# Optimization experiments

Measured on AMD Instinct MI355X. Metric: run time of the kernel, lower is better.

The kernel has to match this reference:

```python
import jax, jax.numpy as jnp
import numpy as np

NF = 64
DG = 8
NB = 5
K = 3
K2 = K * K


def conv2d(x, w, b):
    # x: [B,C,H,W], w: [O,I,3,3] -> SAME padding, stride 1
    y = jax.lax.conv_general_dilated(x, w, (1, 1), 'SAME',
                                     dimension_numbers=('NCHW', 'OIHW', 'NCHW'))
    return y + b[None, :, None, None]


def dcn(x, off_feat, cw, cb, w, b):
    """Modulated deformable conv (DCNv2, extra_offset_mask=True).
    x: [B,C,H,W] sampled input; off_feat: [B,C,H,W] feeds conv_offset_mask.
    cw/cb: offset-mask conv params [3*DG*K2, C, 3, 3]; w/b: main conv [O, C, 3, 3].
    """
    B, C, H, W = x.shape
    Cg = C // DG
    om = conv2d(off_feat, cw, cb)                      # [B, 3*DG*K2, H, W]
    o1, o2, m = jnp.split(om, 3, axis=1)
    dy = o1.reshape(B, DG, K2, H, W)
    dx = o2.reshape(B, DG, K2, H, W)
    mask = jax.nn.sigmoid(m).reshape(B, DG, K2, H, W)
    # kernel tap offsets for 3x3, pad=1, dilation=1
    kyy, kxx = np.meshgrid(np.arange(K) - 1, np.arange(K) - 1, indexing='ij')
    ky = jnp.asarray(kyy.reshape(K2), x.dtype)
    kx = jnp.asarray(kxx.reshape(K2), x.dtype)
    gy = jnp.arange(H, dtype=x.dtype)
    gx = jnp.arange(W, dtype=x.dtype)
    py = gy[None, None, None, :, None] + ky[None, None, :, None, None] + dy  # [B,DG,K2,H,W]
    px = gx[None, None, None, None, :] + kx[None, None, :, None, None] + dx
    y0 = jnp.floor(py)
    x0 = jnp.floor(px)
    wy = py - y0
    wx = px - x0
    y0i = y0.astype(jnp.int32)
    x0i = x0.astype(jnp.int32)
    xg = x.reshape(B, DG, Cg, H * W)

    def gather(iy, ix):
        valid = ((iy >= 0) & (iy < H) & (ix >= 0) & (ix < W)).astype(x.dtype)
        lin = (jnp.clip(iy, 0, H - 1) * W + jnp.clip(ix, 0, W - 1)).reshape(B, DG, 1, K2 * H * W)
        v = jnp.take_along_axis(xg, jnp.broadcast_to(lin, (B, DG, Cg, K2 * H * W)), axis=3)
        return v.reshape(B, DG, Cg, K2, H, W) * valid[:, :, None]

    v00 = gather(y0i, x0i)
    v01 = gather(y0i, x0i + 1)
    v10 = gather(y0i + 1, x0i)
    v11 = gather(y0i + 1, x0i + 1)
    wy_ = wy[:, :, None]
    wx_ = wx[:, :, None]
    val = (v00 * (1 - wy_) * (1 - wx_) + v01 * (1 - wy_) * wx_
           + v10 * wy_ * (1 - wx_) + v11 * wy_ * wx_) * mask[:, :, None]  # [B,DG,Cg,K2,H,W]
    wr = w.reshape(w.shape[0], DG, Cg, K2)
    out = jnp.einsum('bgckhw,ogck->bohw', val, wr) + b[None, :, None, None]
    return out


def setup_inputs() -> dict:
    key = jax.random.key(0)
    ks = jax.random.split(key, 16)

    def w_(k, shape, s=0.05):
        return jax.random.normal(k, shape, jnp.float32) * s

    B, N, C, H, W = 4, 5, 1, 128, 128
    inp = {}
    inp['x'] = jax.random.normal(ks[0], (B, N, C, H, W), jnp.float32)
    inp['w_init'] = w_(ks[1], (NF, C, 3, 3))
    inp['b_init'] = jnp.zeros((NF,), jnp.float32)
    inp['res_w1'] = w_(ks[2], (NB, NF, NF, 3, 3))
    inp['res_b1'] = jnp.zeros((NB, NF), jnp.float32)
    inp['res_w2'] = w_(ks[3], (NB, NF, NF, 3, 3))
    inp['res_b2'] = jnp.zeros((NB, NF), jnp.float32)
    inp['w_bn'] = w_(ks[4], (NF, 2 * NF, 3, 3))
    inp['b_bn'] = jnp.zeros((NF,), jnp.float32)
    inp['off_w'] = w_(ks[5], (4, NF, NF, 3, 3))
    inp['off_b'] = jnp.zeros((4, NF), jnp.float32)
    inp['com_w'] = w_(ks[6], (4, 3 * DG * K2, NF, 3, 3), 0.01)
    inp['com_b'] = jnp.zeros((4, 3 * DG * K2), jnp.float32)
    inp['dcn_w'] = w_(ks[7], (4, NF, NF, 3, 3))
    inp['dcn_b'] = jnp.zeros((4, NF), jnp.float32)
    inp['w_rec'] = w_(ks[8], (C, NF, 3, 3))
    inp['b_rec'] = jnp.zeros((C,), jnp.float32)
    return inp


def reference(x, w_init, b_init, res_w1, res_b1, res_w2, res_b2, w_bn, b_bn,
              off_w, off_b, com_w, com_b, dcn_w, dcn_b, w_rec, b_rec):
    B, N, C, H, W = x.shape
    y = x.reshape(B * N, C, H, W)
    out = jax.nn.relu(conv2d(y, w_init, b_init))
    for i in range(NB):  # ResidualBlock_noBN x nb
        h = jax.nn.relu(conv2d(out, res_w1[i], res_b1[i]))
        out = out + conv2d(h, res_w2[i], res_b2[i])
    out = out.reshape(B, N, NF, H, W)
    ref = out[:, N // 2]
    ys = []
    for i in range(N):
        nei = out[:, i]
        fea = conv2d(jnp.concatenate([ref, nei], axis=1), w_bn, b_bn)
        o = conv2d(fea, off_w[0], off_b[0])
        fea = dcn(fea, o, com_w[0], com_b[0], dcn_w[0], dcn_b[0])
        o = conv2d(fea, off_w[1], off_b[1])
        fea = dcn(fea, o, com_w[1], com_b[1], dcn_w[1], dcn_b[1])
        o = conv2d(fea, off_w[2], off_b[2])
        fea = dcn(nei, o, com_w[2], com_b[2], dcn_w[2], dcn_b[2])
        o = conv2d(fea, off_w[3], off_b[3])
        aligned = dcn(fea, o, com_w[3], com_b[3], dcn_w[3], dcn_b[3])
        ys.append(conv2d(aligned, w_rec, b_rec))
    return jnp.concatenate(ys, axis=1)  # [B, N*C, H, W]
```

## Files before the change

### kernel.cpp

```cpp
#include <hip/hip_runtime.h>
#include <hip/hip_bf16.h>

typedef __hip_bfloat16 bf16;
typedef __attribute__((ext_vector_type(8))) short short8;
typedef __attribute__((ext_vector_type(4))) float floatx4;
typedef unsigned short ush;

#define HH 128
#define WW 128
#define HW 16384

__device__ __forceinline__ float b2f(bf16 v){ return __bfloat162float(v); }
__device__ __forceinline__ float bfu2f(ush u){
  union{unsigned int i; float f;} c; c.i = ((unsigned int)u)<<16; return c.f;
}
__device__ __forceinline__ ush f2bfu(float f){
  bf16 h = __float2bfloat16(f);
  return *(ush*)&h;
}

__global__ void detect_dtype(const ush* __restrict__ x, float* __restrict__ flag){
  __shared__ int bad;
  if (threadIdx.x==0) bad = 0;
  __syncthreads();
  for (int j=threadIdx.x; j<4096; j+=256){
    float f = bfu2f(x[j]);
    if (!(fabsf(f) < 1e4f)) atomicOr(&bad, 1);
  }
  __syncthreads();
  if (threadIdx.x==0) flag[0] = bad ? 0.f : 1.f;
}

__global__ void convert_in(const void* __restrict__ src, float* __restrict__ dst, int n,
                           const float* __restrict__ flag){
  int i = blockIdx.x*256 + threadIdx.x;
  if (i >= n) return;
  float v = (flag[0] > 0.5f) ? b2f(((const bf16*)src)[i]) : ((const float*)src)[i];
  dst[i] = v;
}

__global__ void transpose_w(const float* __restrict__ src, float* __restrict__ dst, int Co, int CiK){
  int tid = blockIdx.x*256 + threadIdx.x;
  if (tid >= Co*CiK) return;
  int co = tid / CiK, r = tid - co*CiK;
  dst[(long)r*Co + co] = src[tid];
}

__global__ void pack_w2(const float* __restrict__ src, ush* __restrict__ dst,
                        int Cout, int Cin, int kh, int nOcB){
  int idx = blockIdx.x*256 + threadIdx.x;
  int total = nOcB*36864;
  if (idx >= total) return;
  int ocb = idx / 36864; int r = idx - ocb*36864;
  int c  = r & 7;
  int lx = (r>>3) & 15;
  int n  = (r>>7) & 3;
  int lk = (r>>9) & 3;
  int j  = r>>11;
  int t = j>>1, ch = j&1;
  int oc = n*16+lx;
  int k = ch*32 + lk*8 + c;
  int ocg = ocb*64 + oc, icg = kh*64 + k;
  float v = (ocg < Cout && icg < Cin) ? src[((long)ocg*Cin + icg)*9 + t] : 0.f;
  dst[idx] = f2bfu(v);
}

__global__ void pack_dcn_w(const float* __restrict__ src, ush* __restrict__ dst){
  int idx = blockIdx.x*256 + threadIdx.x;
  if (idx >= 49152) return;
  int g = idx / 6144; int r = idx - g*6144;
  int oc = r / 96; int k = r - oc*96;
  float v = 0.f;
  if (k < 72){
    int tap = k >> 3, c = k & 7;
    v = src[((long)oc*64 + g*8 + c)*9 + tap];
  }
  dst[idx] = f2bfu(v);
}

__global__ __launch_bounds__(256) void conv_init_kernel(const float* __restrict__ x,
    const float* __restrict__ wT, const float* __restrict__ bias,
    ush* __restrict__ fh, ush* __restrict__ fl){
  __shared__ ush L[256*66];
  int tid = threadIdx.x;
  int tx = tid & 15, ty = tid >> 4;
  int gx = blockIdx.x*16+tx, gy = blockIdx.y*16+ty;
  int n = blockIdx.z;
  const float* xp = x + (long)n*HW;
  float v[9];
  #pragma unroll
  for (int dy=0;dy<3;dy++)
    #pragma unroll
    for (int dx=0;dx<3;dx++){
      int yy = gy+dy-1, xx = gx+dx-1;
      bool ok = (yy>=0)&&(yy<HH)&&(xx>=0)&&(xx<WW);
      v[dy*3+dx] = ok ? xp[yy*WW+xx] : 0.f;
    }
  float acc[64];
  #pragma unroll 1
  for (int oc=0; oc<64; oc++){
    float a = bias[oc];
    #pragma unroll
    for (int k=0;k<9;k++) a = fmaf(v[k], wT[k*64+oc], a);
    acc[oc] = fmaxf(a, 0.f);
  }
  #pragma unroll 1
  for (int pass=0; pass<2; pass++){
    #pragma unroll 1
    for (int oc=0; oc<64; oc++){
      float a = acc[oc];
      ush h = f2bfu(a);
      L[tid*66+oc] = pass ? f2bfu(a - bfu2f(h)) : h;
    }
    __syncthreads();
    ush* dst = pass ? fl : fh;
    for (int j=tid; j<2048; j+=256){
      int c8 = j&7, pidx = j>>3;
      int row = pidx>>4, col = pidx&15;
      long addr = ((long)n*HW + (blockIdx.y*16+row)*WW + blockIdx.x*16+col)*64 + c8*8;
      *(short8*)(dst+addr) = *(const short8*)(L + pidx*66 + c8*8);
    }
    __syncthreads();
  }
}

template<int NPL, int MINW, int MT>
__global__ __launch_bounds__(256, MINW) void conv_mfma(
    const ush* __restrict__ in_hi, const ush* __restrict__ in_lo, long in_ps,
    const ush* __restrict__ in2_hi, const ush* __restrict__ in2_lo, long in2_ps,
    const ush* __restrict__ wpack, const ush* __restrict__ wpack2,
    const float* __restrict__ bias, int has_bias,
    const ush* __restrict__ add_hi, const ush* __restrict__ add_lo,
    long add_ps, int add_cs,
    ush* __restrict__ out_hi, ush* __restrict__ out_lo,
    long out_ps, int out_cs,
    ush* __restrict__ out_pb, int pf_C,
    int Cout, int nOcB, int relu)
{
  constexpr int ROWS = 4*MT + 2;
  constexpr int APX  = ROWS*18;
  constexpr int NPX  = 4*MT*16;
  constexpr int LDSN = (NPL*APX*64 > 2*NPX*66) ? NPL*APX*64 : 2*NPX*66;
  __shared__ ush A[LDSN];
  int tid = threadIdx.x;
  int z = blockIdx.z; int img = z / nOcB; int ocb = z - img*nOcB;
  int x0 = blockIdx.x*16 - 1, y0 = blockIdx.y*(4*MT) - 1;
  int w = tid>>6, l = tid&63, lx = l&15, lk = l>>4;
  floatx4 acc[MT][4];
  #pragma unroll
  for (int mt=0;mt<MT;mt++)
    #pragma unroll
    for (int n=0;n<4;n++) acc[mt][n] = (floatx4){0.f,0.f,0.f,0.f};

  auto phase = [&](const ush* ihb, const ush* ilb, const ush* wfb){
    __syncthreads();
    #pragma unroll
    for (int p=0;p<NPL;p++){
      const ush* src = p ? ilb : ihb;
      ush* dstp = A + p*APX*64;
      for (int j=tid; j<APX*8; j+=256){
        int pidx = j>>3, c8 = j&7;
        int row = pidx/18, col = pidx - row*18;
        int yy = y0+row, xx = x0+col;
        uint4 v = make_uint4(0u,0u,0u,0u);
        if ((unsigned)yy < 128u && (unsigned)xx < 128u)
          v = *(const uint4*)(src + ((long)(yy*WW+xx))*64 + c8*8);
        *(uint4*)(dstp + pidx*64 + ((c8 ^ (pidx&7))<<3)) = v;
      }
    }
    const ush* wfrag = wfb + lk*4*128 + lx*8;
    short8 bf[4][4];
    #pragma unroll
    for (int s=0;s<3;s++)
      #pragma unroll
      for (int n=0;n<4;n++)
        bf[s][n] = *(const short8*)(wfrag + (s*16 + n)*128);
    __syncthreads();
    #pragma unroll
    for (int j=0;j<18;j++){
      int t = j>>1, ch = j&1;
      if (j<15){
        #pragma unroll
        for (int n=0;n<4;n++)
          bf[(j+3)&3][n] = *(const short8*)(wfrag + ((j+3)*16 + n)*128);
      }
      int ky = t/3, kx = t - ky*3;
      int jc = ch*4 + lk;
      #pragma unroll
      for (int mt=0; mt<MT; mt++){
        int pidx = (w*MT+mt+ky)*18 + lx + kx;
        #pragma unroll
        for (int p=0;p<NPL;p++){
          short8 af = *(const short8*)(A + p*APX*64 + pidx*64 + ((jc ^ (pidx&7))<<3));
          #pragma unroll
          for (int n=0;n<4;n++)
            acc[mt][n] = __builtin_amdgcn_mfma_f32_16x16x32_bf16(af, bf[j&3][n], acc[mt][n], 0,0,0);
        }
      }
    }
  };
  phase(in_hi + (long)img*in_ps*64, in_lo + (long)img*in_ps*64,
        wpack + (long)ocb*36864);
  if (wpack2)
    phase(in2_hi + (long)img*in2_ps*64, in2_lo + (long)img*in2_ps*64,
          wpack2 + (long)ocb*36864);

  int ybase = blockIdx.y*(4*MT) + w*MT;
  int xbase = blockIdx.x*16 + lk*4;
  if (out_pb){
    #pragma unroll
    for (int mt=0;mt<MT;mt++){
      int y = ybase + mt;
      #pragma unroll
      for (int n=0;n<4;n++){
        int ocg = ocb*64 + n*16 + lx;
        if (ocg < Cout){
          float bv = has_bias ? bias[ocg] : 0.f;
          #pragma unroll
          for (int r=0;r<4;r++){
            int xg = xbase + r;
            out_pb[((long)img*pf_C + ocg)*HW + y*WW + xg] = f2bfu(acc[mt][n][r] + bv);
          }
        }
      }
    }
  } else {
    __syncthreads();
    ush* L0 = A;
    ush* L1 = A + NPX*66;
    #pragma unroll
    for (int mt=0;mt<MT;mt++){
      int y = ybase + mt;
      int rowl = w*MT + mt;
      #pragma unroll
      for (int n=0;n<4;n++){
        int ocg = n*16 + lx;
        float bv = has_bias ? bias[ocg] : 0.f;
        #pragma unroll
        for (int r=0;r<4;r++){
          int coll = lk*4 + r;
          float v = acc[mt][n][r] + bv;
          if (add_hi){
            long ap = ((long)img*add_ps + y*WW + blockIdx.x*16 + coll)*add_cs + ocg;
            v += bfu2f(add_hi[ap]) + bfu2f(add_lo[ap]);
          }
          if (relu) v = fmaxf(v, 0.f);
          ush h = f2bfu(v);
          L0[(rowl*16+coll)*66 + ocg] = h;
          if (out_lo) L1[(rowl*16+coll)*66 + ocg] = f2bfu(v - bfu2f(h));
        }
      }
    }
    __syncthreads();
    for (int j=tid; j<NPX*8; j+=256){
      int pidx = j>>3, c8 = j&7;
      int row = pidx>>4, col = pidx&15;
      long pp = (long)img*out_ps + (blockIdx.y*(4*MT)+row)*WW + blockIdx.x*16+col;
      *(short8*)(out_hi + pp*64 + c8*8) = *(const short8*)(L0 + pidx*66 + c8*8);
      if (out_lo)
        *(short8*)(out_lo + pp*64 + c8*8) = *(const short8*)(L1 + pidx*66 + c8*8);
    }
  }
}

__global__ __launch_bounds__(256,4) void res_fused(
    const ush* __restrict__ src_h, const ush* __restrict__ src_l,
    const ush* __restrict__ w1, const float* __restrict__ b1,
    const ush* __restrict__ w2, const float* __restrict__ b2,
    ush* __restrict__ dst_h, ush* __restrict__ dst_l)
{
  __shared__ ush F[180*64];
  __shared__ ush Hs[112*64];
  int tid = threadIdx.x;
  int bx = blockIdx.x, by = blockIdx.y, img = blockIdx.z;
  int fy0 = by*4 - 2, fx0 = bx*16 - 2;
  int w = tid>>6, l = tid&63, lx = l&15, lk = l>>4;
  const ush* sh = src_h + (long)img*HW*64;
  for (int j=tid; j<1440; j+=256){
    int pidx = j>>3, c8 = j&7;
    int row = pidx/20, col = pidx - row*20;
    int yy = fy0+row, xx = fx0+col;
    uint4 v = make_uint4(0u,0u,0u,0u);
    if ((unsigned)yy<128u && (unsigned)xx<128u)
      v = *(const uint4*)(sh + ((long)(yy*WW+xx))*64 + c8*8);
    *(uint4*)(F + pidx*64 + ((c8 ^ (pidx&7))<<3)) = v;
  }
  const ush* wf1 = w1 + lk*4*128 + lx*8;
  int hrow[2], hcol[2], hvalid[2];
  #pragma unroll
  for (int mm=0;mm<2;mm++){
    int m = w + mm*4;
    hvalid[mm] = (m < 7);
    int hp = m*16 + lx;
    hrow[mm] = hp/18; hcol[mm] = hp - hrow[mm]*18;
  }
  floatx4 acc1[2][4];
  #pragma unroll
  for (int mm=0;mm<2;mm++)
    #pragma unroll
    for (int n=0;n<4;n++) acc1[mm][n] = (floatx4){0.f,0.f,0.f,0.f};
  short8 bf[4][4];
  #pragma unroll
  for (int s=0;s<3;s++)
    #pragma unroll
    for (int n=0;n<4;n++)
      bf[s][n] = *(const short8*)(wf1 + (s*16 + n)*128);
  __syncthreads();
  #pragma unroll
  for (int j=0;j<18;j++){
    int t = j>>1, ch = j&1;
    if (j<15){
      #pragma unroll
      for (int n=0;n<4;n++)
        bf[(j+3)&3][n] = *(const short8*)(wf1 + ((j+3)*16 + n)*128);
    }
    int ky = t/3, kx = t - ky*3;
    int jc = ch*4 + lk;
    #pragma unroll
    for (int mm=0;mm<2;mm++){
      if (!hvalid[mm]) continue;
      int pidx = (hrow[mm]+ky)*20 + hcol[mm] + kx;
      short8 af = *(const short8*)(F + pidx*64 + ((jc ^ (pidx&7))<<3));
      #pragma unroll
      for (int n=0;n<4;n++)
        acc1[mm][n] = __builtin_amdgcn_mfma_f32_16x16x32_bf16(af, bf[j&3][n], acc1[mm][n], 0,0,0);
    }
  }
  #pragma unroll
  for (int mm=0;mm<2;mm++){
    if (!hvalid[mm]) continue;
    int m = w + mm*4;
    #pragma unroll
    for (int n=0;n<4;n++){
      int oc = n*16+lx;
      float bv = b1[oc];
      #pragma unroll
      for (int r=0;r<4;r++){
        int hp = m*16 + lk*4 + r;
        int hr = hp/18, hc = hp - hr*18;
        int fy = fy0 + 1 + hr, fx = fx0 + 1 + hc;
        bool inimg = ((unsigned)fy < 128u) && ((unsigned)fx < 128u);
        float v = inimg ? fmaxf(acc1[mm][n][r] + bv, 0.f) : 0.f;
        Hs[hp*64 + (((oc>>3) ^ (hp&7))<<3) + (oc&7)] = f2bfu(v);
      }
    }
  }
  __syncthreads();
  const ush* wf2 = w2 + lk*4*128 + lx*8;
  floatx4 acc2[4];
  #pragma unroll
  for (int n=0;n<4;n++) acc2[n] = (floatx4){0.f,0.f,0.f,0.f};
  #pragma unroll
  for (int s=0;s<3;s++)
    #pragma unroll
    for (int n=0;n<4;n++)
      bf[s][n] = *(const short8*)(wf2 + (s*16 + n)*128);
  #pragma unroll
  for (int j=0;j<18;j++){
    int t = j>>1, ch = j&1;
    if (j<15){
      #pragma unroll
      for (int n=0;n<4;n++)
        bf[(j+3)&3][n] = *(const short8*)(wf2 + ((j+3)*16 + n)*128);
    }
    int ky = t/3, kx = t - ky*3;
    int jc = ch*4 + lk;
    int pidx = (w+ky)*18 + lx + kx;
    short8 af = *(const short8*)(Hs + pidx*64 + ((jc ^ (pidx&7))<<3));
    #pragma unroll
    for (int n=0;n<4;n++)
      acc2[n] = __builtin_amdgcn_mfma_f32_16x16x32_bf16(af, bf[j&3][n], acc2[n], 0,0,0);
  }
  const ush* sl = src_l + (long)img*HW*64;
  int gy = by*4 + w;
  float vout[4][4];
  #pragma unroll
  for (int n=0;n<4;n++){
    int oc = n*16+lx;
    float bv = b2[oc];
    #pragma unroll
    for (int r=0;r<4;r++){
      int colp = lk*4 + r;
      int gx = bx*16 + colp;
      int pt = (w+2)*20 + colp + 2;
      float fh = bfu2f(F[pt*64 + (((oc>>3) ^ (pt&7))<<3) + (oc&7)]);
      float fl = bfu2f(sl[((long)(gy*WW+gx))*64 + oc]);
      vout[n][r] = acc2[n][r] + bv + fh + fl;
    }
  }
  __syncthreads();
  ush* L0 = F;
  ush* L1 = F + 64*66;
  #pragma unroll
  for (int n=0;n<4;n++){
    int oc = n*16+lx;
    #pragma unroll
    for (int r=0;r<4;r++){
      int px = w*16 + lk*4 + r;
      float v = vout[n][r];
      ush h = f2bfu(v);
      L0[px*66 + oc] = h;
      L1[px*66 + oc] = f2bfu(v - bfu2f(h));
    }
  }
  __syncthreads();
  for (int j=tid; j<512; j+=256){
    int pidx = j>>3, c8 = j&7;
    int row = pidx>>4, col = pidx&15;
    long pp = ((long)img*HW + (by*4+row)*WW + bx*16+col)*64 + c8*8;
    *(short8*)(dst_h + pp) = *(const short8*)(L0 + pidx*66 + c8*8);
    *(short8*)(dst_l + pp) = *(const short8*)(L1 + pidx*66 + c8*8);
  }
}

__global__ __launch_bounds__(256) void repack_gp(const ush* __restrict__ in_h,
    const ush* __restrict__ in_l, long in_ps, ush* __restrict__ gp){
  long idx = (long)blockIdx.x*256 + threadIdx.x;
  int img = (int)(idx >> 17);
  int rem = (int)(idx & 131071);
  int pix = rem >> 3, c8 = rem & 7;
  long src = ((long)img*in_ps + pix)*64 + c8*8;
  short8 h = *(const short8*)(in_h+src);
  short8 lo = *(const short8*)(in_l+src);
  short8 o;
  #pragma unroll
  for (int c=0;c<8;c++) o[c] = (short)f2bfu(bfu2f((ush)h[c]) + bfu2f((ush)lo[c]));
  *(short8*)(gp + (((long)(img*8+c8))*HW + pix)*8) = o;
}

__global__ __launch_bounds__(256) void dcn_mfma(
    const ush* __restrict__ gp,
    const ush* __restrict__ om,
    const ush* __restrict__ wpk,
    const float* __restrict__ bias,
    ush* __restrict__ out_hi, ush* __restrict__ out_lo)
{
  __shared__ ush S[13312];
  ush* Ah = S;
  ush* Bt = S + 6656;
  int tid = threadIdx.x;
  int half = blockIdx.x, gy = blockIdx.y, img = blockIdx.z;
  int xoff = half*64;
  {
    short8 z = {0,0,0,0,0,0,0,0};
    for (int j=tid; j<192; j+=256){
      int px = j/3, c = j - px*3;
      *(short8*)(Ah + px*104 + 72 + c*8) = z;
    }
  }
  int w = tid>>6, l = tid&63, lx = l&15, lk = l>>4;
  int px_s = tid & 63, q = tid >> 6;
  int t0 = (q==0)?0:(q*2+1), t1 = t0 + ((q==0)?3:2);
  const ush* omb = om + (long)img*216*HW + gy*WW + xoff + px_s;
  floatx4 acc[4];
  #pragma unroll
  for (int n=0;n<4;n++) acc[n] = (floatx4){0.f,0.f,0.f,0.f};

  #pragma unroll 1
  for (int g=0; g<8; g++){
    __syncthreads();
    const ush* wsrc = wpk + g*6144;
    for (int j=tid; j<768; j+=256){
      int oc = j/12, kc = j - oc*12;
      *(short8*)(Bt + oc*104 + kc*8) = *(const short8*)(wsrc + oc*96 + kc*8);
    }
    const ush* gpb = gp + ((long)(img*8+g))*HW*8;
    #pragma unroll 1
    for (int t=t0; t<t1; t++){
      int ch = g*9+t;
      float dy = bfu2f(omb[(long)ch*HW]);
      float dx = bfu2f(omb[(long)(72+ch)*HW]);
      float mv = bfu2f(omb[(long)(144+ch)*HW]);
      float m = 1.f/(1.f+__expf(-mv));
      float py = (float)gy + (float)(t/3 - 1) + dy;
      float pxf = (float)(xoff + px_s) + (float)(t%3 - 1) + dx;
      float fy = floorf(py), fx = floorf(pxf);
      int y0 = (int)fy, x0 = (int)fx;
      float wy = py - fy, wx = pxf - fx;
      bool y0v = (y0>=0 && y0<HH), y1v = (y0+1>=0 && y0+1<HH);
      bool x0v = (x0>=0 && x0<WW), x1v = (x0+1>=0 && x0+1<WW);
      float w00 = (1.f-wy)*(1.f-wx)*m * ((y0v&&x0v)?1.f:0.f);
      float w01 = (1.f-wy)*wx*m      * ((y0v&&x1v)?1.f:0.f);
      float w10 = wy*(1.f-wx)*m      * ((y1v&&x0v)?1.f:0.f);
      float w11 = wy*wx*m            * ((y1v&&x1v)?1.f:0.f);
      int y0c = min(max(y0,0),HH-1), y1c = min(max(y0+1,0),HH-1);
      int x0c = min(max(x0,0),WW-1), x1c = min(max(x0+1,0),WW-1);
      short8 s00 = *(const short8*)(gpb + (((long)(y0c*WW+x0c))<<3));
      short8 s01 = *(const short8*)(gpb + (((long)(y0c*WW+x1c))<<3));
      short8 s10 = *(const short8*)(gpb + (((long)(y1c*WW+x0c))<<3));
      short8 s11 = *(const short8*)(gpb + (((long)(y1c*WW+x1c))<<3));
      short8 vh;
      #pragma unroll
      for (int c=0;c<8;c++){
        float val = w00*bfu2f((ush)s00[c]) + w01*bfu2f((ush)s01[c])
                  + w10*bfu2f((ush)s10[c]) + w11*bfu2f((ush)s11[c]);
        vh[c] = (short)f2bfu(val);
      }
      *(short8*)(Ah + px_s*104 + t*8) = vh;
    }
    __syncthreads();
    #pragma unroll
    for (int ks=0; ks<3; ks++){
      short8 bfg[4];
      #pragma unroll
      for (int n=0;n<4;n++)
        bfg[n] = *(const short8*)(Bt + (n*16+lx)*104 + ks*32 + lk*8);
      int px = w*16 + lx;
      short8 ah = *(const short8*)(Ah + px*104 + ks*32 + lk*8);
      #pragma unroll
      for (int n=0;n<4;n++)
        acc[n] = __builtin_amdgcn_mfma_f32_16x16x32_bf16(ah, bfg[n], acc[n], 0,0,0);
    }
  }
  __syncthreads();
  ush* L0 = S;
  ush* L1 = S + 64*66;
  #pragma unroll
  for (int n=0;n<4;n++){
    int oc = n*16 + lx;
    float bv = bias[oc];
    #pragma unroll
    for (int r=0;r<4;r++){
      int pxl = w*16 + lk*4 + r;
      float v = acc[n][r] + bv;
      ush h = f2bfu(v);
      L0[pxl*66 + oc] = h;
      L1[pxl*66 + oc] = f2bfu(v - bfu2f(h));
    }
  }
  __syncthreads();
  long base = ((long)img*HW + gy*WW + xoff)*64;
  for (int j=tid; j<512; j+=256){
    int pidx = j>>3, c8 = j&7;
    *(short8*)(out_hi + base + pidx*64 + c8*8) = *(const short8*)(L0 + pidx*66 + c8*8);
    *(short8*)(out_lo + base + pidx*64 + c8*8) = *(const short8*)(L1 + pidx*66 + c8*8);
  }
}

__global__ __launch_bounds__(256) void rec_kernel(
    const ush* __restrict__ fh, const ush* __restrict__ fl,
    const float* __restrict__ wT, const float* __restrict__ bias,
    void* __restrict__ out, int ni, const float* __restrict__ flag){
  __shared__ float red[256];
  int tid = threadIdx.x;
  int p = tid & 31, q = tid >> 5;
  int gx = blockIdx.x*32 + p;
  int gy = blockIdx.y;
  int b = blockIdx.z;
  float acc = 0.f;
  #pragma unroll
  for (int t=0;t<9;t++){
    int yy = gy + t/3 - 1, xx = gx + t%3 - 1;
    if (yy<0||yy>=HH||xx<0||xx>=WW) continue;
    long base = ((long)b*HW + yy*WW + xx)*64 + q*8;
    short8 h = *(const short8*)(fh + base);
    short8 lo = *(const short8*)(fl + base);
    #pragma unroll
    for (int cc=0;cc<8;cc++){
      float v = bfu2f((ush)h[cc]) + bfu2f((ush)lo[cc]);
      acc = fmaf(v, wT[(q*8+cc)*9 + t], acc);
    }
  }
  red[q*32+p] = acc;
  __syncthreads();
  if (tid < 32){
    float s = bias[0];
    #pragma unroll
    for (int k=0;k<8;k++) s += red[k*32+tid];
    long idx = ((long)b*5+ni)*HW + gy*WW + blockIdx.x*32 + tid;
    if (flag[0] > 0.5f) ((bf16*)out)[idx] = __float2bfloat16(s);
    else                ((float*)out)[idx] = s;
  }
}

extern "C" void kernel_launch(void* const* d_in, const int* in_sizes, int n_in,
                              void* d_out, int out_size, void* d_ws, size_t ws_size,
                              hipStream_t stream) {
  float* ws = (float*)d_ws;

  size_t off = 16;
  auto alloc = [&](size_t nel){ size_t o = off; off += (nel + 7) & ~(size_t)7; return o; };

  static const int IN_N[17] = {327680, 576, 64, 184320, 320, 184320, 320,
                               73728, 64, 147456, 256, 497664, 864, 147456,
                               256, 576, 1};
  size_t cin[17];
  for (int i=0;i<17;i++) cin[i] = alloc(IN_N[i]);

  size_t wt_init = alloc(640);
  size_t wdcn_pk[4]; for (int s=0;s<4;s++) wdcn_pk[s] = alloc(24576);
  size_t wt_rec = alloc(640);
  size_t pk_res1[5], pk_res2[5];
  for (int i=0;i<5;i++) pk_res1[i] = alloc(18432);
  for (int i=0;i<5;i++) pk_res2[i] = alloc(18432);
  size_t pk_bn[2]; for (int h=0;h<2;h++) pk_bn[h] = alloc(18432);
  size_t pk_off[4]; for (int s=0;s<4;s++) pk_off[s] = alloc(18432);
  size_t pk_com[4]; for (int s=0;s<4;s++) pk_com[s] = alloc(73728);

  size_t feat_h_o = alloc(10485760);
  size_t feat_l_o = alloc(10485760);
  size_t U = alloc(26738688);

  ush* feat_h = (ush*)(ws + feat_h_o);
  ush* feat_l = (ush*)(ws + feat_l_o);
  ush* alt_h  = (ush*)(ws + U);
  ush* alt_l  = (ush*)(ws + U + 10485760);
  ush* hbuf_h = (ush*)(ws + U + 10485760);
  ush* feaA_h = (ush*)(ws + U);
  ush* feaA_l = (ush*)(ws + U + 2097152);
  ush* feaB_h = (ush*)(ws + U + 4194304);
  ush* feaB_l = (ush*)(ws + U + 6291456);
  ush* obuf_h = (ush*)(ws + U + 8388608);
  ush* gpbuf  = (ush*)(ws + U + 10485760);
  ush* ombuf  = (ush*)(ws + U + 12582912);

  float* flag = ws;

  detect_dtype<<<dim3(1), dim3(256), 0, stream>>>((const ush*)d_in[0], flag);
  for (int i=0;i<17;i++){
    int n = IN_N[i];
    convert_in<<<dim3((n+255)/256), dim3(256), 0, stream>>>(d_in[i], ws+cin[i], n, flag);
  }
  const float* b_init = ws+cin[2];
  const float* res_b1 = ws+cin[4];
  const float* res_b2 = ws+cin[6];
  const float* b_bn   = ws+cin[8];
  const float* off_b  = ws+cin[10];
  const float* com_b  = ws+cin[12];
  const float* dcn_b  = ws+cin[14];
  const float* b_rec  = ws+cin[16];

  auto tr = [&](size_t src_o, size_t dst_o, int Co, int CiK){
    int total = Co*CiK;
    transpose_w<<<dim3((total+255)/256), dim3(256), 0, stream>>>(ws+src_o, ws+dst_o, Co, CiK);
  };
  tr(cin[1], wt_init, 64, 9);
  tr(cin[15], wt_rec, 1, 576);
  for (int s=0;s<4;s++)
    pack_dcn_w<<<dim3(192), dim3(256), 0, stream>>>(ws+cin[13]+(size_t)s*36864,
                                                    (ush*)(ws+wdcn_pk[s]));

  auto pack = [&](size_t src_o, size_t dst_o, int Cout, int Cin, int kh, int nOcB){
    int total = nOcB*36864;
    pack_w2<<<dim3((total+255)/256), dim3(256), 0, stream>>>(
        ws+src_o, (ush*)(ws+dst_o), Cout, Cin, kh, nOcB);
  };
  for (int i=0;i<5;i++) pack(cin[3]+(size_t)i*36864, pk_res1[i], 64, 64, 0, 1);
  for (int i=0;i<5;i++) pack(cin[5]+(size_t)i*36864, pk_res2[i], 64, 64, 0, 1);
  for (int h=0;h<2;h++) pack(cin[7], pk_bn[h], 64, 128, h, 1);
  for (int s=0;s<4;s++) pack(cin[9]+(size_t)s*36864,  pk_off[s], 64, 64, 0, 1);
  for (int s=0;s<4;s++) pack(cin[11]+(size_t)s*124416, pk_com[s], 216, 64, 0, 4);

  dim3 cblk(256);
  auto conv = [&](const ush* in_h, const ush* in_l, long in_ps,
                  const ush* in2_h, const ush* in2_l, long in2_ps,
                  size_t pk, const ush* pk2p,
                  const float* bias, int has_bias,
                  const ush* add_h, const ush* add_l, long add_ps, int add_cs,
                  ush* o_h, ush* o_l, long out_ps, int out_cs,
                  ush* o_pb, int pf_C,
                  int Cout, int nOcB, int relu, int N, int nPl, int mtMode){
    if (nPl == 2 && mtMode == 2)
      conv_mfma<2,2,2><<<dim3(8,16,N*nOcB), cblk, 0, stream>>>(
          in_h, in_l, in_ps, in2_h, in2_l, in2_ps,
          (const ush*)(ws+pk), pk2p, bias, has_bias,
          add_h, add_l, add_ps, add_cs, o_h, o_l, out_ps, out_cs,
          o_pb, pf_C, Cout, nOcB, relu);
    else if (nPl == 2 && mtMode == 1)
      conv_mfma<2,2,1><<<dim3(8,32,N*nOcB), cblk, 0, stream>>>(
          in_h, in_l, in_ps, in2_h, in2_l, in2_ps,
          (const ush*)(ws+pk), pk2p, bias, has_bias,
          add_h, add_l, add_ps, add_cs, o_h, o_l, out_ps, out_cs,
          o_pb, pf_C, Cout, nOcB, relu);
    else if (nPl == 1 && mtMode == 1)
      conv_mfma<1,3,1><<<dim3(8,32,N*nOcB), cblk, 0, stream>>>(
          in_h, in_l, in_ps, in2_h, in2_l, in2_ps,
          (const ush*)(ws+pk), pk2p, bias, has_bias,
          add_h, add_l, add_ps, add_cs, o_h, o_l, out_ps, out_cs,
          o_pb, pf_C, Cout, nOcB, relu);
    else
      conv_mfma<1,3,2><<<dim3(8,16,N*nOcB), cblk, 0, stream>>>(
          in_h, in_l, in_ps, in2_h, in2_l, in2_ps,
          (const ush*)(ws+pk), pk2p, bias, has_bias,
          add_h, add_l, add_ps, add_cs, o_h, o_l, out_ps, out_cs,
          o_pb, pf_C, Cout, nOcB, relu);
  };

  conv_init_kernel<<<dim3(8,8,20), cblk, 0, stream>>>(ws+cin[0], ws+wt_init, b_init,
                                                      feat_h, feat_l);
  conv(feat_h, feat_l, HW, nullptr, nullptr, 0, pk_res1[0], nullptr,
       res_b1, 1,
       nullptr, nullptr, 0, 0, hbuf_h, nullptr, HW, 64, nullptr, 0, 64, 1, 1, 20, 2, 1);
  conv(hbuf_h, hbuf_h, HW, nullptr, nullptr, 0, pk_res2[0], nullptr,
       res_b2, 1,
       feat_h, feat_l, HW, 64, feat_h, feat_l, HW, 64, nullptr, 0, 64, 1, 0, 20, 1, 1);
  {
    ush *sh = feat_h, *sl = feat_l, *dh = alt_h, *dl = alt_l;
    for (int i=1;i<5;i++){
      res_fused<<<dim3(8,32,20), cblk, 0, stream>>>(
          sh, sl, (const ush*)(ws+pk_res1[i]), res_b1+(size_t)i*64,
          (const ush*)(ws+pk_res2[i]), res_b2+(size_t)i*64, dh, dl);
      ush* t;
      t = sh; sh = dh; dh = t;
      t = sl; sl = dl; dl = t;
    }
  }
  for (int i=0;i<5;i++){
    conv(feat_h + (size_t)2*HW*64, feat_l + (size_t)2*HW*64, 5L*HW,
         feat_h + (size_t)i*HW*64, feat_l + (size_t)i*HW*64, 5L*HW,
         pk_bn[0], (const ush*)(ws+pk_bn[1]), b_bn, 1,
         nullptr, nullptr, 0, 0, feaA_h, feaA_l, HW, 64, nullptr, 0, 64, 1, 0, 4, 2, 1);
    ush *fa_h = feaA_h, *fa_l = feaA_l, *fb_h = feaB_h, *fb_l = feaB_l;
    for (int s=0;s<4;s++){
      conv(fa_h, fa_h, HW, nullptr, nullptr, 0, pk_off[s], nullptr,
           off_b+(size_t)s*64, 1,
           nullptr, nullptr, 0, 0, obuf_h, nullptr, HW, 64, nullptr, 0, 64, 1, 0, 4, 1, 1);
      conv(obuf_h, obuf_h, HW, nullptr, nullptr, 0, pk_com[s], nullptr,
           com_b+(size_t)s*216, 1,
           nullptr, nullptr, 0, 0, nullptr, nullptr, 0, 0, ombuf, 216, 216, 4, 0, 4, 1, 2);
      const ush *xs_h, *xs_l; long xps;
      if (s == 2){ xs_h = feat_h + (size_t)i*HW*64; xs_l = feat_l + (size_t)i*HW*64; xps = 5L*HW; }
      else       { xs_h = fa_h;                     xs_l = fa_l;                     xps = HW; }
      repack_gp<<<dim3(2048), cblk, 0, stream>>>(xs_h, xs_l, xps, gpbuf);
      dcn_mfma<<<dim3(2,128,4), cblk, 0, stream>>>(gpbuf, ombuf,
          (const ush*)(ws+wdcn_pk[s]), dcn_b+(size_t)s*64, fb_h, fb_l);
      ush* t;
      t = fa_h; fa_h = fb_h; fb_h = t;
      t = fa_l; fa_l = fb_l; fb_l = t;
    }
    rec_kernel<<<dim3(4,128,4), cblk, 0, stream>>>(fa_h, fa_l, ws+wt_rec, b_rec, d_out, i, flag);
  }
}
```

Before: 3.002 ms.

## Fuse gather-layout repack into producer epilogues and batch weight-prep launches

```diff
diff --git a/kernel.cpp b/kernel.cpp
--- a/kernel.cpp
+++ b/kernel.cpp
@@ -31,12 +31,17 @@
   if (threadIdx.x==0) flag[0] = bad ? 0.f : 1.f;
 }
 
-__global__ void convert_in(const void* __restrict__ src, float* __restrict__ dst, int n,
-                           const float* __restrict__ flag){
-  int i = blockIdx.x*256 + threadIdx.x;
-  if (i >= n) return;
-  float v = (flag[0] > 0.5f) ? b2f(((const bf16*)src)[i]) : ((const float*)src)[i];
-  dst[i] = v;
+struct CvtArgs { const void* src[17]; int dst[17]; };
+__global__ void convert_all(CvtArgs a, float* __restrict__ ws, const float* __restrict__ flag){
+  static const int N[17] = {327680, 576, 64, 184320, 320, 184320, 320,
+                            73728, 64, 147456, 256, 497664, 864, 147456,
+                            256, 576, 1};
+  int i = blockIdx.y;
+  int idx = blockIdx.x*256 + threadIdx.x;
+  if (idx >= N[i]) return;
+  float v = (flag[0] > 0.5f) ? b2f(((const bf16*)a.src[i])[idx])
+                             : ((const float*)a.src[i])[idx];
+  ws[a.dst[i] + idx] = v;
 }
 
 __global__ void transpose_w(const float* __restrict__ src, float* __restrict__ dst, int Co, int CiK){
@@ -46,11 +51,17 @@
   dst[(long)r*Co + co] = src[tid];
 }
 
-__global__ void pack_w2(const float* __restrict__ src, ush* __restrict__ dst,
-                        int Cout, int Cin, int kh, int nOcB){
+struct PackArgs { int src[20]; int dst[20]; short Cout[20]; short Cin[20];
+                  short kh[20]; short nOcB[20]; };
+__global__ void pack_all(PackArgs a, const float* __restrict__ ws, ush* __restrict__ wsu){
+  int jb = blockIdx.y;
   int idx = blockIdx.x*256 + threadIdx.x;
+  int nOcB = a.nOcB[jb];
   int total = nOcB*36864;
   if (idx >= total) return;
+  const float* src = ws + a.src[jb];
+  ush* dst = wsu + 2*(size_t)a.dst[jb];
+  int Cout = a.Cout[jb], Cin = a.Cin[jb], kh = a.kh[jb];
   int ocb = idx / 36864; int r = idx - ocb*36864;
   int c  = r & 7;
   int lx = (r>>3) & 15;
@@ -65,7 +76,10 @@
   dst[idx] = f2bfu(v);
 }
 
-__global__ void pack_dcn_w(const float* __restrict__ src, ush* __restrict__ dst){
+__global__ void pack_dcn_w(const float* __restrict__ src0, ush* __restrict__ dst0){
+  int s = blockIdx.y;
+  const float* src = src0 + (long)s*36864;
+  ush* dst = dst0 + (long)s*49152;
   int idx = blockIdx.x*256 + threadIdx.x;
   if (idx >= 49152) return;
   int g = idx / 6144; int r = idx - g*6144;
@@ -135,6 +149,7 @@
     ush* __restrict__ out_hi, ush* __restrict__ out_lo,
     long out_ps, int out_cs,
     ush* __restrict__ out_pb, int pf_C,
+    ush* __restrict__ gp_out,
     int Cout, int nOcB, int relu)
 {
   constexpr int ROWS = 4*MT + 2;
@@ -255,10 +270,21 @@
     for (int j=tid; j<NPX*8; j+=256){
       int pidx = j>>3, c8 = j&7;
       int row = pidx>>4, col = pidx&15;
-      long pp = (long)img*out_ps + (blockIdx.y*(4*MT)+row)*WW + blockIdx.x*16+col;
-      *(short8*)(out_hi + pp*64 + c8*8) = *(const short8*)(L0 + pidx*66 + c8*8);
-      if (out_lo)
-        *(short8*)(out_lo + pp*64 + c8*8) = *(const short8*)(L1 + pidx*66 + c8*8);
+      long pix = (blockIdx.y*(4*MT)+row)*WW + blockIdx.x*16+col;
+      long pp = (long)img*out_ps + pix;
+      short8 h8 = *(const short8*)(L0 + pidx*66 + c8*8);
+      *(short8*)(out_hi + pp*64 + c8*8) = h8;
+      if (out_lo){
+        short8 l8 = *(const short8*)(L1 + pidx*66 + c8*8);
+        *(short8*)(out_lo + pp*64 + c8*8) = l8;
+        if (gp_out){
+          short8 g;
+          #pragma unroll
+          for (int c=0;c<8;c++)
+            g[c] = (short)f2bfu(bfu2f((ush)h8[c]) + bfu2f((ush)l8[c]));
+          *(short8*)(gp_out + (((long)(img*8+c8))*HW + pix)*8) = g;
+        }
+      }
     }
   }
 }
@@ -433,7 +459,8 @@
     const ush* __restrict__ om,
     const ush* __restrict__ wpk,
     const float* __restrict__ bias,
-    ush* __restrict__ out_hi, ush* __restrict__ out_lo)
+    ush* __restrict__ out_hi, ush* __restrict__ out_lo,
+    ush* __restrict__ gp_out)
 {
   __shared__ ush S[13312];
   ush* Ah = S;
@@ -532,8 +559,17 @@
   long base = ((long)img*HW + gy*WW + xoff)*64;
   for (int j=tid; j<512; j+=256){
     int pidx = j>>3, c8 = j&7;
-    *(short8*)(out_hi + base + pidx*64 + c8*8) = *(const short8*)(L0 + pidx*66 + c8*8);
-    *(short8*)(out_lo + base + pidx*64 + c8*8) = *(const short8*)(L1 + pidx*66 + c8*8);
+    short8 h8 = *(const short8*)(L0 + pidx*66 + c8*8);
+    short8 l8 = *(const short8*)(L1 + pidx*66 + c8*8);
+    *(short8*)(out_hi + base + pidx*64 + c8*8) = h8;
+    *(short8*)(out_lo + base + pidx*64 + c8*8) = l8;
+    if (gp_out){
+      short8 g8;
+      #pragma unroll
+      for (int c=0;c<8;c++)
+        g8[c] = (short)f2bfu(bfu2f((ush)h8[c]) + bfu2f((ush)l8[c]));
+      *(short8*)(gp_out + (((long)(img*8+c8))*HW + gy*WW + xoff + pidx)*8) = g8;
+    }
   }
 }
 
@@ -611,15 +647,17 @@
   ush* feaB_h = (ush*)(ws + U + 4194304);
   ush* feaB_l = (ush*)(ws + U + 6291456);
   ush* obuf_h = (ush*)(ws + U + 8388608);
-  ush* gpbuf  = (ush*)(ws + U + 10485760);
+  ush* gpA    = (ush*)(ws + U + 10485760);
   ush* ombuf  = (ush*)(ws + U + 12582912);
+  ush* gpB    = (ush*)(ws + U + 19660800);
 
   float* flag = ws;
 
   detect_dtype<<<dim3(1), dim3(256), 0, stream>>>((const ush*)d_in[0], flag);
-  for (int i=0;i<17;i++){
-    int n = IN_N[i];
-    convert_in<<<dim3((n+255)/256), dim3(256), 0, stream>>>(d_in[i], ws+cin[i], n, flag);
+  {
+    CvtArgs ca;
+    for (int i=0;i<17;i++){ ca.src[i] = d_in[i]; ca.dst[i] = (int)cin[i]; }
+    convert_all<<<dim3(1945,17), dim3(256), 0, stream>>>(ca, ws, flag);
   }
   const float* b_init = ws+cin[2];
   const float* res_b1 = ws+cin[4];
@@ -630,26 +668,24 @@
   const float* dcn_b  = ws+cin[14];
   const float* b_rec  = ws+cin[16];
 
-  auto tr = [&](size_t src_o, size_t dst_o, int Co, int CiK){
-    int total = Co*CiK;
-    transpose_w<<<dim3((total+255)/256), dim3(256), 0, stream>>>(ws+src_o, ws+dst_o, Co, CiK);
-  };
-  tr(cin[1], wt_init, 64, 9);
-  tr(cin[15], wt_rec, 1, 576);
-  for (int s=0;s<4;s++)
-    pack_dcn_w<<<dim3(192), dim3(256), 0, stream>>>(ws+cin[13]+(size_t)s*36864,
-                                                    (ush*)(ws+wdcn_pk[s]));
-
-  auto pack = [&](size_t src_o, size_t dst_o, int Cout, int Cin, int kh, int nOcB){
-    int total = nOcB*36864;
-    pack_w2<<<dim3((total+255)/256), dim3(256), 0, stream>>>(
-        ws+src_o, (ush*)(ws+dst_o), Cout, Cin, kh, nOcB);
-  };
-  for (int i=0;i<5;i++) pack(cin[3]+(size_t)i*36864, pk_res1[i], 64, 64, 0, 1);
-  for (int i=0;i<5;i++) pack(cin[5]+(size_t)i*36864, pk_res2[i], 64, 64, 0, 1);
-  for (int h=0;h<2;h++) pack(cin[7], pk_bn[h], 64, 128, h, 1);
-  for (int s=0;s<4;s++) pack(cin[9]+(size_t)s*36864,  pk_off[s], 64, 64, 0, 1);
-  for (int s=0;s<4;s++) pack(cin[11]+(size_t)s*124416, pk_com[s], 216, 64, 0, 4);
+  transpose_w<<<dim3(3), dim3(256), 0, stream>>>(ws+cin[1], ws+wt_init, 64, 9);
+  transpose_w<<<dim3(3), dim3(256), 0, stream>>>(ws+cin[15], ws+wt_rec, 1, 576);
+  pack_dcn_w<<<dim3(192,4), dim3(256), 0, stream>>>(ws+cin[13], (ush*)(ws+wdcn_pk[0]));
+  {
+    PackArgs pa;
+    int j = 0;
+    for (int i=0;i<5;i++){ pa.src[j]=(int)(cin[3]+(size_t)i*36864); pa.dst[j]=(int)pk_res1[i];
+      pa.Cout[j]=64; pa.Cin[j]=64; pa.kh[j]=0; pa.nOcB[j]=1; j++; }
+    for (int i=0;i<5;i++){ pa.src[j]=(int)(cin[5]+(size_t)i*36864); pa.dst[j]=(int)pk_res2[i];
+      pa.Cout[j]=64; pa.Cin[j]=64; pa.kh[j]=0; pa.nOcB[j]=1; j++; }
+    for (int h=0;h<2;h++){ pa.src[j]=(int)cin[7]; pa.dst[j]=(int)pk_bn[h];
+      pa.Cout[j]=64; pa.Cin[j]=128; pa.kh[j]=(short)h; pa.nOcB[j]=1; j++; }
+    for (int s=0;s<4;s++){ pa.src[j]=(int)(cin[9]+(size_t)s*36864); pa.dst[j]=(int)pk_off[s];
+      pa.Cout[j]=64; pa.Cin[j]=64; pa.kh[j]=0; pa.nOcB[j]=1; j++; }
+    for (int s=0;s<4;s++){ pa.src[j]=(int)(cin[11]+(size_t)s*124416); pa.dst[j]=(int)pk_com[s];
+      pa.Cout[j]=216; pa.Cin[j]=64; pa.kh[j]=0; pa.nOcB[j]=4; j++; }
+    pack_all<<<dim3(576,20), dim3(256), 0, stream>>>(pa, ws, (ush*)ws);
+  }
 
   dim3 cblk(256);
   auto conv = [&](const ush* in_h, const ush* in_l, long in_ps,
@@ -658,42 +694,42 @@
                   const float* bias, int has_bias,
                   const ush* add_h, const ush* add_l, long add_ps, int add_cs,
                   ush* o_h, ush* o_l, long out_ps, int out_cs,
-                  ush* o_pb, int pf_C,
+                  ush* o_pb, int pf_C, ush* gp_o,
                   int Cout, int nOcB, int relu, int N, int nPl, int mtMode){
     if (nPl == 2 && mtMode == 2)
       conv_mfma<2,2,2><<<dim3(8,16,N*nOcB), cblk, 0, stream>>>(
           in_h, in_l, in_ps, in2_h, in2_l, in2_ps,
           (const ush*)(ws+pk), pk2p, bias, has_bias,
           add_h, add_l, add_ps, add_cs, o_h, o_l, out_ps, out_cs,
-          o_pb, pf_C, Cout, nOcB, relu);
+          o_pb, pf_C, gp_o, Cout, nOcB, relu);
     else if (nPl == 2 && mtMode == 1)
       conv_mfma<2,2,1><<<dim3(8,32,N*nOcB), cblk, 0, stream>>>(
           in_h, in_l, in_ps, in2_h, in2_l, in2_ps,
           (const ush*)(ws+pk), pk2p, bias, has_bias,
           add_h, add_l, add_ps, add_cs, o_h, o_l, out_ps, out_cs,
-          o_pb, pf_C, Cout, nOcB, relu);
+          o_pb, pf_C, gp_o, Cout, nOcB, relu);
     else if (nPl == 1 && mtMode == 1)
       conv_mfma<1,3,1><<<dim3(8,32,N*nOcB), cblk, 0, stream>>>(
           in_h, in_l, in_ps, in2_h, in2_l, in2_ps,
           (const ush*)(ws+pk), pk2p, bias, has_bias,
           add_h, add_l, add_ps, add_cs, o_h, o_l, out_ps, out_cs,
-          o_pb, pf_C, Cout, nOcB, relu);
+          o_pb, pf_C, gp_o, Cout, nOcB, relu);
     else
       conv_mfma<1,3,2><<<dim3(8,16,N*nOcB), cblk, 0, stream>>>(
           in_h, in_l, in_ps, in2_h, in2_l, in2_ps,
           (const ush*)(ws+pk), pk2p, bias, has_bias,
           add_h, add_l, add_ps, add_cs, o_h, o_l, out_ps, out_cs,
-          o_pb, pf_C, Cout, nOcB, relu);
+          o_pb, pf_C, gp_o, Cout, nOcB, relu);
   };
 
   conv_init_kernel<<<dim3(8,8,20), cblk, 0, stream>>>(ws+cin[0], ws+wt_init, b_init,
                                                       feat_h, feat_l);
   conv(feat_h, feat_l, HW, nullptr, nullptr, 0, pk_res1[0], nullptr,
        res_b1, 1,
-       nullptr, nullptr, 0, 0, hbuf_h, nullptr, HW, 64, nullptr, 0, 64, 1, 1, 20, 2, 1);
+       nullptr, nullptr, 0, 0, hbuf_h, nullptr, HW, 64, nullptr, 0, nullptr, 64, 1, 1, 20, 2, 1);
   conv(hbuf_h, hbuf_h, HW, nullptr, nullptr, 0, pk_res2[0], nullptr,
        res_b2, 1,
-       feat_h, feat_l, HW, 64, feat_h, feat_l, HW, 64, nullptr, 0, 64, 1, 0, 20, 1, 1);
+       feat_h, feat_l, HW, 64, feat_h, feat_l, HW, 64, nullptr, 0, nullptr, 64, 1, 0, 20, 1, 1);
   {
     ush *sh = feat_h, *sl = feat_l, *dh = alt_h, *dl = alt_l;
     for (int i=1;i<5;i++){
@@ -709,21 +745,22 @@
     conv(feat_h + (size_t)2*HW*64, feat_l + (size_t)2*HW*64, 5L*HW,
          feat_h + (size_t)i*HW*64, feat_l + (size_t)i*HW*64, 5L*HW,
          pk_bn[0], (const ush*)(ws+pk_bn[1]), b_bn, 1,
-         nullptr, nullptr, 0, 0, feaA_h, feaA_l, HW, 64, nullptr, 0, 64, 1, 0, 4, 2, 1);
+         nullptr, nullptr, 0, 0, feaA_h, feaA_l, HW, 64, nullptr, 0, gpA, 64, 1, 0, 4, 2, 1);
     ush *fa_h = feaA_h, *fa_l = feaA_l, *fb_h = feaB_h, *fb_l = feaB_l;
     for (int s=0;s<4;s++){
       conv(fa_h, fa_h, HW, nullptr, nullptr, 0, pk_off[s], nullptr,
            off_b+(size_t)s*64, 1,
-           nullptr, nullptr, 0, 0, obuf_h, nullptr, HW, 64, nullptr, 0, 64, 1, 0, 4, 1, 1);
+           nullptr, nullptr, 0, 0, obuf_h, nullptr, HW, 64, nullptr, 0, nullptr, 64, 1, 0, 4, 1, 1);
       conv(obuf_h, obuf_h, HW, nullptr, nullptr, 0, pk_com[s], nullptr,
            com_b+(size_t)s*216, 1,
-           nullptr, nullptr, 0, 0, nullptr, nullptr, 0, 0, ombuf, 216, 216, 4, 0, 4, 1, 2);
-      const ush *xs_h, *xs_l; long xps;
-      if (s == 2){ xs_h = feat_h + (size_t)i*HW*64; xs_l = feat_l + (size_t)i*HW*64; xps = 5L*HW; }
-      else       { xs_h = fa_h;                     xs_l = fa_l;                     xps = HW; }
-      repack_gp<<<dim3(2048), cblk, 0, stream>>>(xs_h, xs_l, xps, gpbuf);
-      dcn_mfma<<<dim3(2,128,4), cblk, 0, stream>>>(gpbuf, ombuf,
-          (const ush*)(ws+wdcn_pk[s]), dcn_b+(size_t)s*64, fb_h, fb_l);
+           nullptr, nullptr, 0, 0, nullptr, nullptr, 0, 0, ombuf, 216, nullptr, 216, 4, 0, 4, 1, 2);
+      if (s == 2)
+        repack_gp<<<dim3(2048), cblk, 0, stream>>>(feat_h + (size_t)i*HW*64,
+            feat_l + (size_t)i*HW*64, 5L*HW, gpA);
+      const ush* gp_src = (s==0) ? gpA : (s==1) ? gpB : (s==2) ? gpA : gpB;
+      ush* gp_dst = (s==0 || s==2) ? gpB : nullptr;
+      dcn_mfma<<<dim3(2,128,4), cblk, 0, stream>>>(gp_src, ombuf,
+          (const ush*)(ws+wdcn_pk[s]), dcn_b+(size_t)s*64, fb_h, fb_l, gp_dst);
       ush* t;
       t = fa_h; fa_h = fb_h; fb_h = t;
       t = fa_l; fa_l = fb_l; fb_l = t;
```

Measured after the change: 2.931 ms. 2.4% less time.
